# Kernel tuning notes

Hardware: AMD Instinct MI355X
Metric: run time of the kernel (lower is better)

Reference implementation:

```python
import jax, jax.numpy as jnp
import numpy as np

NUM_ITERATIONS = 3
NUM_ROUTES = 6912  # 32*6*6*6


def _squash(t):
    # t: [..., O]; squash along last dim
    sq = jnp.sum(t * t, axis=-1, keepdims=True)
    return sq * t / ((1.0 + sq) * jnp.sqrt(sq))


def setup_inputs() -> dict:
    key = jax.random.key(0)
    k1, k2 = jax.random.split(key)
    B, R, I, C, O = 64, NUM_ROUTES, 8, 10, 16
    x = jax.random.normal(k1, (B, R, I), dtype=jnp.float32)
    route_weights = jax.random.normal(k2, (C, R, I, O), dtype=jnp.float32)
    return {"x": x, "route_weights": route_weights}


def reference(x, route_weights):
    # x: [B, R, I]; route_weights: [C, R, I, O]
    # priors = x[None,:,:,None,:] @ W[:,None,:,:,:] -> [C, B, R, 1, O]
    priors = jnp.einsum('bri,crio->cbro', x, route_weights)[:, :, :, None, :]
    logits = jnp.zeros_like(priors)  # [C, B, R, 1, O]
    outputs = None
    for i in range(NUM_ITERATIONS):
        # softmax over routes (dim=2), matching custom softmax(input, dim=2)
        probs = jax.nn.softmax(logits, axis=2)
        outputs = _squash(jnp.sum(probs * priors, axis=2, keepdims=True))  # [C,B,1,1,O]
        if i != NUM_ROUTES - 1:  # always true in original (num_routes >> iters)
            delta = jnp.sum(priors * outputs, axis=-1, keepdims=True)  # [C,B,R,1,1]
            logits = logits + delta
    return outputs
```

## Files before the change

kernel.cpp:

```cpp
#include <hip/hip_runtime.h>
#include <math.h>

#define BB 64
#define RR 6912
#define II 8
#define CC 10
#define OO 16
#define RPB2 96
#define NCH2 72
#define NG2 12
#define NBLK 720
#define MRG_PAD 20
#define WTILE_I4 (RPB2*16)
#define MRGF (4*64*MRG_PAD + 4*64)
#define PWW (CC*NCH2*BB*OO)
#define PZW (CC*NCH2*BB)
#define L_ARR(c)      ((c) * 32)
#define L_ARREP(c,r)  ((10 + (c)*8 + (r)) * 32)
#define L_CD(c)       ((90 + (c)) * 32)
#define L_RD(c,r)     ((100 + (c)*8 + (r)) * 32)
#define FLAGI (180*32)

typedef _Float16 h2 __attribute__((ext_vector_type(2)));
typedef _Float16 half8 __attribute__((ext_vector_type(8)));
typedef float f32x16 __attribute__((ext_vector_type(16)));
union HV { int4 v; h2 h[4]; half8 h8; };

__device__ __forceinline__ void xchf(float* p, float v) {
    float old = __hip_atomic_exchange(p, v, __ATOMIC_RELAXED, __HIP_MEMORY_SCOPE_AGENT);
    asm volatile("" :: "v"(old));
}
__device__ __forceinline__ void xchf2(float* p, float a, float b) {
    union { unsigned long long u; float f[2]; } v;
    v.f[0] = a; v.f[1] = b;
    unsigned long long old = __hip_atomic_exchange((unsigned long long*)p, v.u,
                              __ATOMIC_RELAXED, __HIP_MEMORY_SCOPE_AGENT);
    asm volatile("" :: "v"(old));
}
__device__ __forceinline__ int addi(int* p) {
    return __hip_atomic_fetch_add(p, 1, __ATOMIC_RELAXED, __HIP_MEMORY_SCOPE_AGENT);
}
__device__ __forceinline__ void xchi(int* p, int v) {
    int old = __hip_atomic_exchange(p, v, __ATOMIC_RELAXED, __HIP_MEMORY_SCOPE_AGENT);
    asm volatile("" :: "v"(old));
}
template <int SLP, int GUARD>
__device__ __forceinline__ void pollge(const int* p, int tgt) {
    int v = __hip_atomic_load(p, __ATOMIC_RELAXED, __HIP_MEMORY_SCOPE_AGENT);
    int g = 0;
    while (v < tgt && ++g < GUARD) {
        __builtin_amdgcn_s_sleep(SLP);
        v = __hip_atomic_load(p, __ATOMIC_RELAXED, __HIP_MEMORY_SCOPE_AGENT);
    }
}

__global__ __launch_bounds__(256) void prep_kernel(
    const float* __restrict__ x, int4* __restrict__ xth4,
    const float4* __restrict__ w4, int4* __restrict__ wh4,
    int* __restrict__ flags)
{
    __shared__ __align__(16) float4 lds4[64 * 34];
    const int t = threadIdx.x;
    const int bid = blockIdx.x;

    {
        const unsigned idx = (unsigned)bid * 256u + (unsigned)t;
        if (idx < (unsigned)FLAGI) flags[idx] = 0;
    }

    if (bid < 432) {
        const int rblk = bid >> 2;
        const int bblk = bid & 3;
        const int r0 = rblk * 64, b0 = bblk * 16;
        {
            const int rl = t & 63;
            const int bl0 = t >> 6;
#pragma unroll
            for (int kb = 0; kb < 4; ++kb) {
                const int bl = kb * 4 + bl0;
                const float4* src = (const float4*)(x + ((size_t)(b0 + bl) * RR + (r0 + rl)) * II);
                lds4[rl * 34 + bl * 2 + 0] = src[0];
                lds4[rl * 34 + bl * 2 + 1] = src[1];
            }
        }
        __syncthreads();
        {
            const int bl = t & 15;
            const int rw0 = t >> 4;
#pragma unroll
            for (int kr = 0; kr < 4; ++kr) {
                const int rw = kr * 16 + rw0;
                float4 a = lds4[rw * 34 + bl * 2 + 0];
                float4 bq = lds4[rw * 34 + bl * 2 + 1];
                HV u;
                u.h[0] = h2{(_Float16)a.x,  (_Float16)a.y};
                u.h[1] = h2{(_Float16)a.z,  (_Float16)a.w};
                u.h[2] = h2{(_Float16)bq.x, (_Float16)bq.y};
                u.h[3] = h2{(_Float16)bq.z, (_Float16)bq.w};
                xth4[(size_t)(r0 + rw) * BB + (b0 + bl)] = u.v;
            }
        }
    } else {
        _Float16* wl = (_Float16*)lds4;
        const int wblk = bid - 432;
        const int rp = t >> 5;
        const int i  = (t >> 2) & 7;
        const int o0 = (t & 3) * 4;
#pragma unroll 1
        for (int sb = 0; sb < 8; ++sb) {
            const int blk8 = wblk * 8 + sb;
            const float4 v = w4[(size_t)blk8 * 256 + t];
            _Float16* wb = wl + (sb & 1) * 1024;
            wb[(rp * 16 + o0 + 0) * 8 + i] = (_Float16)v.x;
            wb[(rp * 16 + o0 + 1) * 8 + i] = (_Float16)v.y;
            wb[(rp * 16 + o0 + 2) * 8 + i] = (_Float16)v.z;
            wb[(rp * 16 + o0 + 3) * 8 + i] = (_Float16)v.w;
            __syncthreads();
            if (t < 128) wh4[(size_t)blk8 * 128 + t] = ((const int4*)wb)[t];
        }
    }
}

template <int MODE>
__device__ __forceinline__ void it_phase(
    const int4* __restrict__ xth4, const int4* wlds, float* mrg,
    const float* __restrict__ ov,
    float* __restrict__ pw, float* __restrict__ pz,
    int* flags, int c, int chunk, int xcd, int t, int ph)
{
    const int wv = t >> 6;
    const int l = t & 63;
    const int b = l & 31;
    const int hi = l >> 5;
    const int aquad = (l >> 4) & 1;
    const bool aact = (aquad == hi);

    if (MODE != 0) {
        if (t == 0) pollge<8, (1 << 14)>(flags + L_RD(c, xcd), ph - 1);
        __syncthreads();
    }

    float accA[8], accB[8];
#pragma unroll
    for (int j = 0; j < 8; ++j) { accA[j] = 0.f; accB[j] = 0.f; }
    float ZA = 0.f, ZB = 0.f;

    float ovA[8], ovB[8];
    if (MODE != 0) {
        const float* pa = ov + ((size_t)c * BB + b) * OO + 4 * hi;
        const float* pb = ov + ((size_t)c * BB + 32 + b) * OO + 4 * hi;
        float4 a0 = *(const float4*)(pa);
        float4 a1 = *(const float4*)(pa + 8);
        float4 b0 = *(const float4*)(pb);
        float4 b1 = *(const float4*)(pb + 8);
        ovA[0]=a0.x; ovA[1]=a0.y; ovA[2]=a0.z; ovA[3]=a0.w;
        ovA[4]=a1.x; ovA[5]=a1.y; ovA[6]=a1.z; ovA[7]=a1.w;
        ovB[0]=b0.x; ovB[1]=b0.y; ovB[2]=b0.z; ovB[3]=b0.w;
        ovB[4]=b1.x; ovB[5]=b1.y; ovB[6]=b1.z; ovB[7]=b1.w;
    }

    const int rbase = chunk * RPB2 + wv * 24;

    f32x16 cA, cB, zf;
#pragma unroll
    for (int q = 0; q < 16; ++q) { cA[q] = 0.f; cB[q] = 0.f; zf[q] = 0.f; }

    HV xc0, xc1, xn0, xn1;
    xc0.v = xth4[(size_t)(rbase + hi) * BB + b];
    xc1.v = xth4[(size_t)(rbase + hi) * BB + 32 + b];
    xn0 = xc0; xn1 = xc1;

#pragma unroll 1
    for (int g = 0; g < NG2; ++g) {
        if (g + 1 < NG2) {
            const int rn = rbase + (g + 1) * 2 + hi;
            xn0.v = xth4[(size_t)rn * BB + b];
            xn1.v = xth4[(size_t)rn * BB + 32 + b];
        }
        const int rl0 = wv * 24 + g * 2;
        HV wq;
        wq.v = wlds[(rl0 + aquad) * 16 + (l & 15)];
        if (!aact) wq.v = make_int4(0, 0, 0, 0);

        if (MODE == 0) {
            cA = __builtin_amdgcn_mfma_f32_32x32x16_f16(wq.h8, xc0.h8, cA, 0, 0, 0);
            cB = __builtin_amdgcn_mfma_f32_32x32x16_f16(wq.h8, xc1.h8, cB, 0, 0, 0);
        } else {
            f32x16 p0 = __builtin_amdgcn_mfma_f32_32x32x16_f16(wq.h8, xc0.h8, zf, 0, 0, 0);
            f32x16 p1 = __builtin_amdgcn_mfma_f32_32x32x16_f16(wq.h8, xc1.h8, zf, 0, 0, 0);
            float dA0 = 0.f, dA1 = 0.f, dB0 = 0.f, dB1 = 0.f;
#pragma unroll
            for (int j = 0; j < 8; ++j) {
                dA0 = fmaf(p0[j],     ovA[j], dA0);
                dA1 = fmaf(p0[j + 8], ovA[j], dA1);
                dB0 = fmaf(p1[j],     ovB[j], dB0);
                dB1 = fmaf(p1[j + 8], ovB[j], dB1);
            }
            dA0 += __shfl_xor(dA0, 32);
            dA1 += __shfl_xor(dA1, 32);
            dB0 += __shfl_xor(dB0, 32);
            dB1 += __shfl_xor(dB1, 32);
            const float eA0 = __expf(dA0), eA1 = __expf(dA1);
            const float eB0 = __expf(dB0), eB1 = __expf(dB1);
            ZA += eA0 + eA1; ZB += eB0 + eB1;
#pragma unroll
            for (int j = 0; j < 8; ++j) {
                accA[j] = fmaf(eA0, p0[j], fmaf(eA1, p0[j + 8], accA[j]));
                accB[j] = fmaf(eB0, p1[j], fmaf(eB1, p1[j + 8], accB[j]));
            }
        }
        xc0 = xn0; xc1 = xn1;
    }

    if (MODE == 0) {
#pragma unroll
        for (int j = 0; j < 8; ++j) {
            accA[j] = cA[j] + cA[j + 8];
            accB[j] = cB[j] + cB[j + 8];
        }
    }

    {
        float* m0 = mrg + (wv * 64 + b) * MRG_PAD + 4 * hi;
        *(float4*)(m0)     = make_float4(accA[0], accA[1], accA[2], accA[3]);
        *(float4*)(m0 + 8) = make_float4(accA[4], accA[5], accA[6], accA[7]);
        float* m1 = mrg + (wv * 64 + 32 + b) * MRG_PAD + 4 * hi;
        *(float4*)(m1)     = make_float4(accB[0], accB[1], accB[2], accB[3]);
        *(float4*)(m1 + 8) = make_float4(accB[4], accB[5], accB[6], accB[7]);
        if (MODE != 0 && hi == 0) {
            float* zr = mrg + 4 * 64 * MRG_PAD;
            zr[wv * 64 + b] = ZA;
            zr[wv * 64 + 32 + b] = ZB;
        }
    }
    __syncthreads();

    {
        const int b2 = t >> 2, q = t & 3;
        float4 sum = make_float4(0.f, 0.f, 0.f, 0.f);
#pragma unroll
        for (int w2 = 0; w2 < 4; ++w2) {
            const float4 v = *(const float4*)(mrg + (w2 * 64 + b2) * MRG_PAD + q * 4);
            sum.x += v.x; sum.y += v.y; sum.z += v.z; sum.w += v.w;
        }
        float* dst = pw + (((size_t)(c * NCH2 + chunk) * BB + b2) * OO) + q * 4;
        xchf2(dst + 0, sum.x, sum.y);
        xchf2(dst + 2, sum.z, sum.w);
        if (MODE != 0 && q == 0) {
            const float* zr = mrg + 4 * 64 * MRG_PAD;
            float z = 0.f;
#pragma unroll
            for (int w2 = 0; w2 < 4; ++w2) z += zr[w2 * 64 + b2];
            xchf(pz + (size_t)(c * NCH2 + chunk) * BB + b2, z);
        }
    }

    __syncthreads();
    if (t == 0) {
        const int old = addi(flags + L_ARR(c));
        if (old == NCH2 * ph - 1) {
#pragma unroll
            for (int r = 0; r < 8; ++r) xchi(flags + L_ARREP(c, r), ph);
        }
    }
}

template <int MODE>
__device__ __forceinline__ void combine_phase(
    const float* __restrict__ pw, const float* __restrict__ pzw,
    const float* __restrict__ addv, float* __restrict__ dst, bool coh,
    int* flags, int bid, int t, float* cl, int ph)
{
    const int c2 = bid >> 6, b2 = bid & 63;
    const int o = t & 15, g = t >> 4;

    if (t == 0) pollge<8, (1 << 14)>(flags + L_ARREP(c2, bid & 7), ph);
    __syncthreads();

    const float* base = pw + (size_t)c2 * NCH2 * (BB * OO);
    float s = 0.f, zl = 0.f;
#pragma unroll
    for (int k = 0; k < 5; ++k) {
        const int rid = g + k * 16;
        if (rid < NCH2) {
            s += base[(size_t)rid * (BB * OO) + b2 * OO + o];
            if (MODE != 0 && o == 0)
                zl += pzw[(size_t)c2 * NCH2 * BB + (size_t)rid * BB + b2];
        }
    }
    cl[t] = s;
    if (MODE != 0 && o == 0) cl[256 + g] = zl;
    __syncthreads();

    if (g == 0) {
#pragma unroll
        for (int k = 1; k < 16; ++k) s += cl[k * 16 + o];
        if (MODE != 0) {
            float Zt = 0.f;
#pragma unroll
            for (int k = 0; k < 16; ++k) Zt += cl[256 + k];
            s /= Zt;
        } else {
            s *= (1.0f / RR);
        }
        float sq = s * s;
#pragma unroll
        for (int w = 1; w < 16; w <<= 1) sq += __shfl_xor(sq, w);
        float val = s * sqrtf(sq) / (1.f + sq);
        if (MODE == 1) val += addv[(size_t)bid * OO + o];
        if (coh) xchf(dst + (size_t)bid * OO + o, val);
        else     dst[(size_t)bid * OO + o] = val;
    }
    __syncthreads();

    if (MODE != 2 && t == 0) {
        const int old = addi(flags + L_CD(c2));
        if (old == CC * BB / CC * ph - 1) {
#pragma unroll
            for (int r = 0; r < 8; ++r) xchi(flags + L_RD(c2, r), ph);
        }
    }
}

__global__ __launch_bounds__(256, 3) void fused_kernel(
    const int4* __restrict__ xth4, const int4* __restrict__ wh4,
    float* pw0, float* pw1, float* pw2, float* pz1, float* pz2,
    float* v0, float* outsum, float* out, int* flags)
{
    __shared__ __align__(16) int4 wlds[WTILE_I4];
    __shared__ __align__(16) float mrg[MRGF];
    __shared__ float cl[272];

    const int bid = blockIdx.x;
    const int t = threadIdx.x;
    const int xcd = bid & 7;
    const int u = xcd * 90 + (bid >> 3);
    const int chunk = u / 10;
    const int c = u - chunk * 10;

    {
        const int4* src = wh4 + ((size_t)c * RR + (size_t)chunk * RPB2) * 16;
#pragma unroll
        for (int k = 0; k < 6; ++k) wlds[k * 256 + t] = src[k * 256 + t];
    }
    __syncthreads();

    it_phase<0>(xth4, wlds, mrg, nullptr, pw0, nullptr, flags, c, chunk, xcd, t, 1);
    if (bid < CC * BB) combine_phase<0>(pw0, nullptr, nullptr, v0, true, flags, bid, t, cl, 1);
    it_phase<1>(xth4, wlds, mrg, v0, pw1, pz1, flags, c, chunk, xcd, t, 2);
    if (bid < CC * BB) combine_phase<1>(pw1, pz1, v0, outsum, true, flags, bid, t, cl, 2);
    it_phase<2>(xth4, wlds, mrg, outsum, pw2, pz2, flags, c, chunk, xcd, t, 3);
    if (bid < CC * BB) combine_phase<2>(pw2, pz2, nullptr, out, false, flags, bid, t, cl, 3);
}

extern "C" void kernel_launch(void* const* d_in, const int* in_sizes, int n_in,
                              void* d_out, int out_size, void* d_ws, size_t ws_size,
                              hipStream_t stream)
{
    const float* x = (const float*)d_in[0];
    const float* w = (const float*)d_in[1];
    float* out = (float*)d_out;

    float* ws = (float*)d_ws;
    float* xth    = ws;
    float* wh     = xth + (size_t)RR * BB * 4;
    float* pw0    = wh + (size_t)CC * RR * 64;
    float* pw1    = pw0 + PWW;
    float* pw2    = pw1 + PWW;
    float* pz1    = pw2 + PWW;
    float* pz2    = pz1 + PZW;
    float* v0     = pz2 + PZW;
    float* outsum = v0 + CC * BB * OO;
    int*   flags  = (int*)(outsum + CC * BB * OO);

    int4* xth4 = (int4*)xth;
    int4* wh4  = (int4*)wh;
    const float4* w4 = (const float4*)w;

    prep_kernel<<<dim3(432 + 1080), dim3(256), 0, stream>>>(x, xth4, w4, wh4, flags);
    fused_kernel<<<dim3(NBLK), dim3(256), 0, stream>>>(
        xth4, wh4, pw0, pw1, pw2, pz1, pz2, v0, outsum, out, flags);
}
```

Before: 141.6 us.

## Fuse weight fp16 conversion into main kernel and transpose partial-sum layout

```diff
diff --git a/kernel.cpp b/kernel.cpp
--- a/kernel.cpp
+++ b/kernel.cpp
@@ -56,7 +56,6 @@
 
 __global__ __launch_bounds__(256) void prep_kernel(
     const float* __restrict__ x, int4* __restrict__ xth4,
-    const float4* __restrict__ w4, int4* __restrict__ wh4,
     int* __restrict__ flags)
 {
     __shared__ __align__(16) float4 lds4[64 * 34];
@@ -68,55 +67,35 @@
         if (idx < (unsigned)FLAGI) flags[idx] = 0;
     }
 
-    if (bid < 432) {
-        const int rblk = bid >> 2;
-        const int bblk = bid & 3;
-        const int r0 = rblk * 64, b0 = bblk * 16;
-        {
-            const int rl = t & 63;
-            const int bl0 = t >> 6;
-#pragma unroll
-            for (int kb = 0; kb < 4; ++kb) {
-                const int bl = kb * 4 + bl0;
-                const float4* src = (const float4*)(x + ((size_t)(b0 + bl) * RR + (r0 + rl)) * II);
-                lds4[rl * 34 + bl * 2 + 0] = src[0];
-                lds4[rl * 34 + bl * 2 + 1] = src[1];
-            }
-        }
-        __syncthreads();
-        {
-            const int bl = t & 15;
-            const int rw0 = t >> 4;
-#pragma unroll
-            for (int kr = 0; kr < 4; ++kr) {
-                const int rw = kr * 16 + rw0;
-                float4 a = lds4[rw * 34 + bl * 2 + 0];
-                float4 bq = lds4[rw * 34 + bl * 2 + 1];
-                HV u;
-                u.h[0] = h2{(_Float16)a.x,  (_Float16)a.y};
-                u.h[1] = h2{(_Float16)a.z,  (_Float16)a.w};
-                u.h[2] = h2{(_Float16)bq.x, (_Float16)bq.y};
-                u.h[3] = h2{(_Float16)bq.z, (_Float16)bq.w};
-                xth4[(size_t)(r0 + rw) * BB + (b0 + bl)] = u.v;
-            }
-        }
-    } else {
-        _Float16* wl = (_Float16*)lds4;
-        const int wblk = bid - 432;
-        const int rp = t >> 5;
-        const int i  = (t >> 2) & 7;
-        const int o0 = (t & 3) * 4;
-#pragma unroll 1
-        for (int sb = 0; sb < 8; ++sb) {
-            const int blk8 = wblk * 8 + sb;
-            const float4 v = w4[(size_t)blk8 * 256 + t];
-            _Float16* wb = wl + (sb & 1) * 1024;
-            wb[(rp * 16 + o0 + 0) * 8 + i] = (_Float16)v.x;
-            wb[(rp * 16 + o0 + 1) * 8 + i] = (_Float16)v.y;
-            wb[(rp * 16 + o0 + 2) * 8 + i] = (_Float16)v.z;
-            wb[(rp * 16 + o0 + 3) * 8 + i] = (_Float16)v.w;
-            __syncthreads();
-            if (t < 128) wh4[(size_t)blk8 * 128 + t] = ((const int4*)wb)[t];
+    const int rblk = bid >> 2;
+    const int bblk = bid & 3;
+    const int r0 = rblk * 64, b0 = bblk * 16;
+    {
+        const int rl = t & 63;
+        const int bl0 = t >> 6;
+#pragma unroll
+        for (int kb = 0; kb < 4; ++kb) {
+            const int bl = kb * 4 + bl0;
+            const float4* src = (const float4*)(x + ((size_t)(b0 + bl) * RR + (r0 + rl)) * II);
+            lds4[rl * 34 + bl * 2 + 0] = src[0];
+            lds4[rl * 34 + bl * 2 + 1] = src[1];
+        }
+    }
+    __syncthreads();
+    {
+        const int bl = t & 15;
+        const int rw0 = t >> 4;
+#pragma unroll
+        for (int kr = 0; kr < 4; ++kr) {
+            const int rw = kr * 16 + rw0;
+            float4 a = lds4[rw * 34 + bl * 2 + 0];
+            float4 bq = lds4[rw * 34 + bl * 2 + 1];
+            HV u;
+            u.h[0] = h2{(_Float16)a.x,  (_Float16)a.y};
+            u.h[1] = h2{(_Float16)a.z,  (_Float16)a.w};
+            u.h[2] = h2{(_Float16)bq.x, (_Float16)bq.y};
+            u.h[3] = h2{(_Float16)bq.z, (_Float16)bq.w};
+            xth4[(size_t)(r0 + rw) * BB + (b0 + bl)] = u.v;
         }
     }
 }
@@ -243,7 +222,7 @@
             const float4 v = *(const float4*)(mrg + (w2 * 64 + b2) * MRG_PAD + q * 4);
             sum.x += v.x; sum.y += v.y; sum.z += v.z; sum.w += v.w;
         }
-        float* dst = pw + (((size_t)(c * NCH2 + chunk) * BB + b2) * OO) + q * 4;
+        float* dst = pw + (((size_t)(c * BB + b2) * NCH2 + chunk) * OO) + q * 4;
         xchf2(dst + 0, sum.x, sum.y);
         xchf2(dst + 2, sum.z, sum.w);
         if (MODE != 0 && q == 0) {
@@ -251,7 +230,7 @@
             float z = 0.f;
 #pragma unroll
             for (int w2 = 0; w2 < 4; ++w2) z += zr[w2 * 64 + b2];
-            xchf(pz + (size_t)(c * NCH2 + chunk) * BB + b2, z);
+            xchf(pz + (size_t)(c * BB + b2) * NCH2 + chunk, z);
         }
     }
 
@@ -277,15 +256,15 @@
     if (t == 0) pollge<8, (1 << 14)>(flags + L_ARREP(c2, bid & 7), ph);
     __syncthreads();
 
-    const float* base = pw + (size_t)c2 * NCH2 * (BB * OO);
+    const float* base = pw + (size_t)(c2 * BB + b2) * NCH2 * OO;
+    const float* zb   = pzw + (size_t)(c2 * BB + b2) * NCH2;
     float s = 0.f, zl = 0.f;
 #pragma unroll
     for (int k = 0; k < 5; ++k) {
         const int rid = g + k * 16;
         if (rid < NCH2) {
-            s += base[(size_t)rid * (BB * OO) + b2 * OO + o];
-            if (MODE != 0 && o == 0)
-                zl += pzw[(size_t)c2 * NCH2 * BB + (size_t)rid * BB + b2];
+            s += base[rid * OO + o];
+            if (MODE != 0 && o == 0) zl += zb[rid];
         }
     }
     cl[t] = s;
@@ -315,7 +294,7 @@
 
     if (MODE != 2 && t == 0) {
         const int old = addi(flags + L_CD(c2));
-        if (old == CC * BB / CC * ph - 1) {
+        if (old == 64 * ph - 1) {
 #pragma unroll
             for (int r = 0; r < 8; ++r) xchi(flags + L_RD(c2, r), ph);
         }
@@ -323,7 +302,7 @@
 }
 
 __global__ __launch_bounds__(256, 3) void fused_kernel(
-    const int4* __restrict__ xth4, const int4* __restrict__ wh4,
+    const int4* __restrict__ xth4, const float* __restrict__ w,
     float* pw0, float* pw1, float* pw2, float* pz1, float* pz2,
     float* v0, float* outsum, float* out, int* flags)
 {
@@ -339,9 +318,19 @@
     const int c = u - chunk * 10;
 
     {
-        const int4* src = wh4 + ((size_t)c * RR + (size_t)chunk * RPB2) * 16;
-#pragma unroll
-        for (int k = 0; k < 6; ++k) wlds[k * 256 + t] = src[k * 256 + t];
+        const float4* wsrc = (const float4*)(w + ((size_t)c * RR + (size_t)chunk * RPB2) * 128);
+        _Float16* wl = (_Float16*)wlds;
+        const int i  = (t >> 2) & 7;
+        const int o0 = (t & 3) * 4;
+#pragma unroll 6
+        for (int p = 0; p < 12; ++p) {
+            const float4 v = wsrc[p * 256 + t];
+            const int rp = (p * 256 + t) >> 5;
+            wl[(rp * 16 + o0 + 0) * 8 + i] = (_Float16)v.x;
+            wl[(rp * 16 + o0 + 1) * 8 + i] = (_Float16)v.y;
+            wl[(rp * 16 + o0 + 2) * 8 + i] = (_Float16)v.z;
+            wl[(rp * 16 + o0 + 3) * 8 + i] = (_Float16)v.w;
+        }
     }
     __syncthreads();
 
@@ -363,8 +352,7 @@
 
     float* ws = (float*)d_ws;
     float* xth    = ws;
-    float* wh     = xth + (size_t)RR * BB * 4;
-    float* pw0    = wh + (size_t)CC * RR * 64;
+    float* pw0    = xth + (size_t)RR * BB * 4;
     float* pw1    = pw0 + PWW;
     float* pw2    = pw1 + PWW;
     float* pz1    = pw2 + PWW;
@@ -374,10 +362,8 @@
     int*   flags  = (int*)(outsum + CC * BB * OO);
 
     int4* xth4 = (int4*)xth;
-    int4* wh4  = (int4*)wh;
-    const float4* w4 = (const float4*)w;
-
-    prep_kernel<<<dim3(432 + 1080), dim3(256), 0, stream>>>(x, xth4, w4, wh4, flags);
+
+    prep_kernel<<<dim3(432), dim3(256), 0, stream>>>(x, xth4, flags);
     fused_kernel<<<dim3(NBLK), dim3(256), 0, stream>>>(
-        xth4, wh4, pw0, pw1, pw2, pz1, pz2, v0, outsum, out, flags);
-}
+        xth4, w, pw0, pw1, pw2, pz1, pz2, v0, outsum, out, flags);
+}
```

Result: faster. 133.7 us (-5.6%).
